# Optimization experiments

Hardware: AMD Instinct MI355X
Metric: run time of the kernel (lower is better)

## Reference

```python
import jax, jax.numpy as jnp
import numpy as np

B, T, C = 4, 2048, 1024
N_HEAD = 16
HEAD = C // N_HEAD  # 64


def _rope_tables(T, dim, base=10000.0):
    inv_freq = 1.0 / (base ** (jnp.arange(0, dim, 2, dtype=jnp.float32) / dim))
    t = jnp.arange(T, dtype=jnp.float32)
    freqs = jnp.einsum('i,j->ij', t, inv_freq)           # [T, dim/2]
    emb = jnp.concatenate([freqs, freqs], axis=-1)        # [T, dim]
    return jnp.cos(emb), jnp.sin(emb)                     # each [T, dim]


def _rotate_half(x):
    x1, x2 = x[..., : x.shape[-1] // 2], x[..., x.shape[-1] // 2:]
    return jnp.concatenate([-x2, x1], axis=-1)


def setup_inputs() -> dict:
    key = jax.random.key(0)
    ks = jax.random.split(key, 4)
    x = jax.random.normal(ks[0], (B, T, C), dtype=jnp.float32)
    w_attn = jax.random.normal(ks[1], (C, 3 * C), dtype=jnp.float32) * (1.0 / np.sqrt(C))
    b_attn = jnp.zeros((3 * C,), dtype=jnp.float32)
    w_proj = jax.random.normal(ks[2], (C, C), dtype=jnp.float32) * (1.0 / np.sqrt(C))
    b_proj = jnp.zeros((C,), dtype=jnp.float32)
    return {"x": x, "w_attn": w_attn, "b_attn": b_attn, "w_proj": w_proj, "b_proj": b_proj}


def reference(x, w_attn, b_attn, w_proj, b_proj):
    Bx, Tx, Cx = x.shape
    qkv = x @ w_attn + b_attn                             # [B,T,3C]
    q, k, v = jnp.split(qkv, 3, axis=-1)
    # [B,T,C] -> [B,H,T,hd]
    def to_heads(t):
        return t.reshape(Bx, Tx, N_HEAD, HEAD).transpose(0, 2, 1, 3)
    q, k, v = to_heads(q), to_heads(k), to_heads(v)
    cos, sin = _rope_tables(Tx, HEAD)                     # [T,hd]
    cos = cos[None, None, :, :]
    sin = sin[None, None, :, :]
    q = q * cos + _rotate_half(q) * sin
    k = k * cos + _rotate_half(k) * sin
    scale = 1.0 / np.sqrt(HEAD)
    att = jnp.einsum('bhqd,bhkd->bhqk', q, k) * scale     # [B,H,T,T]
    causal = jnp.tril(jnp.ones((Tx, Tx), dtype=bool))
    att = jnp.where(causal[None, None], att, -jnp.inf)
    att = jax.nn.softmax(att, axis=-1)
    y = jnp.einsum('bhqk,bhkd->bhqd', att, v)             # [B,H,T,hd]
    y = y.transpose(0, 2, 1, 3).reshape(Bx, Tx, Cx)
    return y @ w_proj + b_proj
```

## Files before the change

kernel.cpp:

```cpp
#include <hip/hip_runtime.h>

#define B_  4
#define T_  2048
#define C_  1024
#define NH_ 16
#define HD_ 64
#define BT_ (B_*T_)
#define N3C (3*C_)

typedef _Float16 f16;
typedef _Float16 half8 __attribute__((ext_vector_type(8)));
typedef _Float16 half4 __attribute__((ext_vector_type(4)));
typedef _Float16 half2v __attribute__((ext_vector_type(2)));
typedef float f32x4 __attribute__((ext_vector_type(4)));

__device__ __forceinline__ void gld16(const f16* g, f16* l) {
  __builtin_amdgcn_global_load_lds(
      (const __attribute__((address_space(1))) unsigned int*)g,
      (__attribute__((address_space(3))) unsigned int*)l, 16, 0, 0);
}

__device__ __forceinline__ float fast_exp2(float x) {
#if __has_builtin(__builtin_amdgcn_exp2f)
  return __builtin_amdgcn_exp2f(x);
#else
  return exp2f(x);
#endif
}

__device__ __forceinline__ half2v cvt_pk_f16(float a, float b) {
#if __has_builtin(__builtin_amdgcn_cvt_pkrtz)
  return __builtin_bit_cast(half2v, __builtin_amdgcn_cvt_pkrtz(a, b));
#else
  half2v r; r[0] = (f16)a; r[1] = (f16)b; return r;
#endif
}

__global__ __launch_bounds__(256) void prep(
    const float* __restrict__ X, f16* __restrict__ X16,
    const float* __restrict__ Wa, f16* __restrict__ Wta,
    const float* __restrict__ Wp, f16* __restrict__ Wtp,
    float2* __restrict__ cs)
{
  __shared__ float Ls[64][65];
  const int tid = threadIdx.x;
  const int blk = blockIdx.x;
  if (blk < 4096) {
    const int i = blk * 256 + tid;
    const float4 a = ((const float4*)X)[i * 2];
    const float4 b = ((const float4*)X)[i * 2 + 1];
    half8 hx;
    hx[0] = (f16)a.x; hx[1] = (f16)a.y; hx[2] = (f16)a.z; hx[3] = (f16)a.w;
    hx[4] = (f16)b.x; hx[5] = (f16)b.y; hx[6] = (f16)b.z; hx[7] = (f16)b.w;
    ((half8*)X16)[i] = hx;
    return;
  }
  if (blk >= 5120) {
    const int i = (blk - 5120) * 256 + tid;
    const int f = i & 31, t = i >> 5;
    const float inv = expf(-(2.0f * (float)f / 64.0f) * 9.210340371976184f);
    float sn, cn;
    sincosf((float)t * inv, &sn, &cn);
    cs[i] = make_float2(cn, sn);
    return;
  }
  const float* W; f16* Wt; int N, i2;
  if (blk < 4864) { W = Wa; Wt = Wta; N = N3C; i2 = blk - 4096; }
  else            { W = Wp; Wt = Wtp; N = C_;  i2 = blk - 4864; }
  const int nblk = N >> 6;
  const int n0 = (i2 % nblk) * 64, k0 = (i2 / nblk) * 64;
#pragma unroll
  for (int j = 0; j < 4; ++j) {
    const int idx = j * 256 + tid;
    const int r = idx >> 4, c = (idx & 15) * 4;
    const float4 w = *(const float4*)(W + (size_t)(k0 + r) * N + n0 + c);
    Ls[r][c + 0] = w.x; Ls[r][c + 1] = w.y; Ls[r][c + 2] = w.z; Ls[r][c + 3] = w.w;
  }
  __syncthreads();
#pragma unroll
  for (int j = 0; j < 2; ++j) {
    const int idx = j * 256 + tid;
    const int r = idx >> 3, c = (idx & 7) * 8;
    half8 hw;
#pragma unroll
    for (int u = 0; u < 8; ++u) hw[u] = (f16)Ls[c + u][r];
    *(half8*)(Wt + (size_t)(n0 + r) * C_ + k0 + c) = hw;
  }
}

__global__ __launch_bounds__(256) void gemm_qkv(
    const f16* __restrict__ A, const f16* __restrict__ Bt,
    const float* __restrict__ bias, const float2* __restrict__ cs,
    f16* __restrict__ Qo, f16* __restrict__ Ko, f16* __restrict__ Vt_g)
{
  __shared__ f16 S[16384];
  f16* As = S;
  f16* Bs = S + 8192;
  const int tid  = threadIdx.x;
  const int row0 = blockIdx.y * 128;
  const int col0 = blockIdx.x * 128;
  const int wave = tid >> 6, lane = tid & 63;
  const int l = lane & 15, quad = lane >> 4;
  const int wm = wave >> 1, wn = wave & 1;
  const int sr = tid >> 3;
  const int scs = ((tid & 7) ^ (sr & 7)) * 8;
  const int lq7 = l & 7;

  f32x4 acc[4][4];
#pragma unroll
  for (int mi = 0; mi < 4; ++mi)
#pragma unroll
    for (int ni = 0; ni < 4; ++ni) acc[mi][ni] = (f32x4)0.0f;

  for (int k0 = 0; k0 < C_; k0 += 64) {
    __syncthreads();
#pragma unroll
    for (int p = 0; p < 4; ++p) {
      const int r = p * 32 + sr;
      gld16(A  + (size_t)(row0 + r) * C_ + k0 + scs, &As[p * 2048 + tid * 8]);
      gld16(Bt + (size_t)(col0 + r) * C_ + k0 + scs, &Bs[p * 2048 + tid * 8]);
    }
    __syncthreads();

#pragma unroll
    for (int s = 0; s < 2; ++s) {
      half8 af[4], bf[4];
#pragma unroll
      for (int mi = 0; mi < 4; ++mi)
        af[mi] = *(const half8*)&As[(wm * 64 + mi * 16 + l) * 64 + ((((s << 2) | quad) ^ lq7) << 3)];
#pragma unroll
      for (int ni = 0; ni < 4; ++ni)
        bf[ni] = *(const half8*)&Bs[(wn * 64 + ni * 16 + l) * 64 + ((((s << 2) | quad) ^ lq7) << 3)];
#pragma unroll
      for (int mi = 0; mi < 4; ++mi)
#pragma unroll
        for (int ni = 0; ni < 4; ++ni)
          acc[mi][ni] = __builtin_amdgcn_mfma_f32_16x16x32_f16(af[mi], bf[ni], acc[mi][ni], 0, 0, 0);
    }
  }

  const int region = col0 >> 10;
  const int colw = col0 + wn * 64;
  const int h = (colw & 1023) >> 6;
  if (region < 2) {
    f16* dst = (region == 0) ? Qo : Ko;
    const float qs = (region == 0) ? 0.18033688f : 1.0f;
#pragma unroll
    for (int mi = 0; mi < 4; ++mi) {
#pragma unroll
      for (int r = 0; r < 4; ++r) {
        const int gm = row0 + wm * 64 + mi * 16 + quad * 4 + r;
        const int b = gm >> 11, t = gm & (T_ - 1);
        const size_t base = ((size_t)(b * NH_ + h) * T_ + t) * HD_;
        const float2* csrow = cs + t * 32;
#pragma unroll
        for (int ni = 0; ni < 2; ++ni) {
          const int d = ni * 16 + l;
          const float2 c2 = csrow[d];
          const float x1 = acc[mi][ni][r]     + bias[colw + d];
          const float x2 = acc[mi][ni + 2][r] + bias[colw + d + 32];
          dst[base + d]      = (f16)((x1 * c2.x - x2 * c2.y) * qs);
          dst[base + d + 32] = (f16)((x2 * c2.x + x1 * c2.y) * qs);
        }
      }
    }
  } else {
    __syncthreads();
    const int bloc  = row0 >> 11;
    const int tbase = row0 & (T_ - 1);
#pragma unroll
    for (int mi = 0; mi < 4; ++mi) {
      const int t_loc = wm * 64 + mi * 16 + quad * 4;
#pragma unroll
      for (int ni = 0; ni < 4; ++ni) {
        const int d = ni * 16 + l;
        const float bs = bias[colw + d];
        half4 o;
#pragma unroll
        for (int r = 0; r < 4; ++r) o[r] = (f16)(acc[mi][ni][r] + bs);
        const int ts = t_loc ^ ((d & 15) << 3);
        *(half4*)&S[wn * 8192 + d * 128 + ts] = o;
      }
    }
    __syncthreads();
#pragma unroll
    for (int j = 0; j < 8; ++j) {
      const int flat = j * 256 + tid;
      const int buf  = flat >> 10;
      const int rem  = flat & 1023;
      const int d    = rem >> 4;
      const int tt   = (rem & 15) << 3;
      const half8 v  = *(const half8*)&S[buf * 8192 + d * 128 + (tt ^ ((d & 15) << 3))];
      const int hh   = ((col0 + buf * 64) & 1023) >> 6;
      *(half8*)(Vt_g + ((size_t)((bloc * NH_ + hh) * HD_ + d)) * T_ + tbase + tt) = v;
    }
  }
}

__global__ __launch_bounds__(256) void attn_mfma(
    const f16* __restrict__ Qg, const f16* __restrict__ Kg,
    const f16* __restrict__ Vt_g, f16* __restrict__ Y)
{
  __shared__ f16 Ks[2][64 * 64];
  __shared__ f16 Vt[2][64 * 64];
  const int tid  = threadIdx.x;
  const int w    = (blockIdx.x & 7) * 128 + (blockIdx.x >> 3);
  const int bh   = w >> 4;
  const int pr   = w & 15;
  const int b    = bh >> 4, h = bh & 15;
  const int wave = tid >> 6, lane = tid & 63;
  const int l    = lane & 15, quad = lane >> 4;
  const int lq7  = l & 7;
  const int r0   = tid >> 3, cc = tid & 7;

  const f16* kbase  = Kg   + (size_t)bh * T_ * HD_;
  const f16* vtbase = Vt_g + (size_t)bh * HD_ * T_;

  const int qts[2] = { 31 - pr, pr };

#pragma unroll 1
  for (int pass = 0; pass < 2; ++pass) {
    const int qt   = qts[pass];
    const int nkt  = qt + 1;
    const int qrow = qt * 64 + wave * 16 + l;

    half8 qf[2];
    {
      const f16* qp = Qg + ((size_t)bh * T_ + qrow) * HD_;
      qf[0] = *(const half8*)(qp + quad * 8);
      qf[1] = *(const half8*)(qp + 32 + quad * 8);
    }

    f32x4 O[4];
#pragma unroll
    for (int mi = 0; mi < 4; ++mi) O[mi] = (f32x4)0.0f;
    float l_run = 0.f;
    const f32x4 zz = (f32x4)0.0f;

    half8 hk[2], hv[2];
#pragma unroll
    for (int i = 0; i < 2; ++i) {
      const int r = i * 32 + r0;
      hk[i] = *(const half8*)(kbase + (size_t)r * HD_ + cc * 8);
      hv[i] = *(const half8*)(vtbase + (size_t)r * T_ + cc * 8);
    }

    if (pass == 1) __syncthreads();

    for (int kt = 0; kt < nkt; ++kt) {
      f16* KsB = Ks[kt & 1];
      f16* VtB = Vt[kt & 1];
#pragma unroll
      for (int i = 0; i < 2; ++i) {
        const int r = i * 32 + r0;
        const int cst = ((cc ^ (r & 7)) << 3);
        *(half8*)&KsB[r * 64 + cst] = hk[i];
        *(half8*)&VtB[r * 64 + cst] = hv[i];
      }
      __syncthreads();
      if (kt + 1 < nkt) {
#pragma unroll
        for (int i = 0; i < 2; ++i) {
          const int r = i * 32 + r0;
          hk[i] = *(const half8*)(kbase + (size_t)((kt + 1) * 64 + r) * HD_ + cc * 8);
          hv[i] = *(const half8*)(vtbase + (size_t)r * T_ + (kt + 1) * 64 + cc * 8);
        }
      }

      f32x4 St[4];
#pragma unroll
      for (int st = 0; st < 4; ++st) {
        const int row = st * 16 + l;
        const half8 af0 = *(const half8*)&KsB[row * 64 + (((quad) ^ lq7) << 3)];
        St[st] = __builtin_amdgcn_mfma_f32_16x16x32_f16(af0, qf[0], zz, 0, 0, 0);
        const half8 af1 = *(const half8*)&KsB[row * 64 + (((4 | quad) ^ lq7) << 3)];
        St[st] = __builtin_amdgcn_mfma_f32_16x16x32_f16(af1, qf[1], St[st], 0, 0, 0);
      }

      const bool domask = (kt == qt);
      const int k0 = kt * 64;
      half4 pf[4];
      float psum = 0.f;
#pragma unroll
      for (int st = 0; st < 4; ++st) {
        float pv[4];
#pragma unroll
        for (int r = 0; r < 4; ++r) {
          float x = St[st][r];
          if (domask) {
            const int key = k0 + st * 16 + quad * 4 + r;
            if (key > qrow) x = -1e9f;
          }
          const float ev = fast_exp2(x);
          pv[r] = ev;
          psum += ev;
        }
        const half2v lo = cvt_pk_f16(pv[0], pv[1]);
        const half2v hi = cvt_pk_f16(pv[2], pv[3]);
        pf[st][0] = lo[0]; pf[st][1] = lo[1];
        pf[st][2] = hi[0]; pf[st][3] = hi[1];
      }
      l_run += psum;

#pragma unroll
      for (int mi = 0; mi < 4; ++mi) {
        const int row = mi * 16 + l;
#pragma unroll
        for (int ki = 0; ki < 4; ++ki) {
          const int kch = (ki << 1) | (quad >> 1);
          const half4 vf = *(const half4*)&VtB[row * 64 + ((kch ^ lq7) << 3) + ((quad & 1) << 2)];
          O[mi] = __builtin_amdgcn_mfma_f32_16x16x16f16(vf, pf[ki], O[mi], 0, 0, 0);
        }
      }
    }

    float lt = l_run;
    lt += __shfl_xor(lt, 16);
    lt += __shfl_xor(lt, 32);
    const float inv = 1.0f / lt;
    f16* yp = Y + ((size_t)(b * T_) + qrow) * C_ + h * 64;
#pragma unroll
    for (int mi = 0; mi < 4; ++mi) {
      half4 o;
      o[0] = (f16)(O[mi][0] * inv); o[1] = (f16)(O[mi][1] * inv);
      o[2] = (f16)(O[mi][2] * inv); o[3] = (f16)(O[mi][3] * inv);
      *(half4*)(yp + mi * 16 + quad * 4) = o;
    }
  }
}

__global__ __launch_bounds__(256) void gemm_proj(
    const f16* __restrict__ A, const f16* __restrict__ Bt,
    const float* __restrict__ bias, float* __restrict__ Out)
{
  __shared__ f16 As[128 * 64];
  __shared__ f16 Bs[128 * 64];
  const int tid  = threadIdx.x;
  const int row0 = blockIdx.y * 128;
  const int col0 = blockIdx.x * 128;
  const int wave = tid >> 6, lane = tid & 63;
  const int l = lane & 15, quad = lane >> 4;
  const int wm = wave >> 1, wn = wave & 1;
  const int sr = tid >> 3;
  const int scs = ((tid & 7) ^ (sr & 7)) * 8;
  const int lq7 = l & 7;

  f32x4 acc[4][4];
#pragma unroll
  for (int mi = 0; mi < 4; ++mi)
#pragma unroll
    for (int ni = 0; ni < 4; ++ni) acc[mi][ni] = (f32x4)0.0f;

  for (int k0 = 0; k0 < C_; k0 += 64) {
    __syncthreads();
#pragma unroll
    for (int p = 0; p < 4; ++p) {
      const int r = p * 32 + sr;
      gld16(A  + (size_t)(row0 + r) * C_ + k0 + scs, &As[p * 2048 + tid * 8]);
      gld16(Bt + (size_t)(col0 + r) * C_ + k0 + scs, &Bs[p * 2048 + tid * 8]);
    }
    __syncthreads();

#pragma unroll
    for (int s = 0; s < 2; ++s) {
      half8 af[4], bf[4];
#pragma unroll
      for (int mi = 0; mi < 4; ++mi)
        af[mi] = *(const half8*)&As[(wm * 64 + mi * 16 + l) * 64 + ((((s << 2) | quad) ^ lq7) << 3)];
#pragma unroll
      for (int ni = 0; ni < 4; ++ni)
        bf[ni] = *(const half8*)&Bs[(wn * 64 + ni * 16 + l) * 64 + ((((s << 2) | quad) ^ lq7) << 3)];
#pragma unroll
      for (int mi = 0; mi < 4; ++mi)
#pragma unroll
        for (int ni = 0; ni < 4; ++ni)
          acc[mi][ni] = __builtin_amdgcn_mfma_f32_16x16x32_f16(af[mi], bf[ni], acc[mi][ni], 0, 0, 0);
    }
  }

#pragma unroll
  for (int mi = 0; mi < 4; ++mi) {
#pragma unroll
    for (int ni = 0; ni < 4; ++ni) {
#pragma unroll
      for (int r = 0; r < 4; ++r) {
        const int gm = row0 + wm * 64 + mi * 16 + quad * 4 + r;
        const int n  = col0 + wn * 64 + ni * 16 + l;
        Out[(size_t)gm * C_ + n] = acc[mi][ni][r] + bias[n];
      }
    }
  }
}

extern "C" void kernel_launch(void* const* d_in, const int* in_sizes, int n_in,
                              void* d_out, int out_size, void* d_ws, size_t ws_size,
                              hipStream_t stream) {
  const float* x      = (const float*)d_in[0];
  const float* w_attn = (const float*)d_in[1];
  const float* b_attn = (const float*)d_in[2];
  const float* w_proj = (const float*)d_in[3];
  const float* b_proj = (const float*)d_in[4];
  float* out = (float*)d_out;

  const size_t elems = (size_t)BT_ * C_;
  f16* x16 = (f16*)d_ws;
  f16* wta = x16 + elems;
  f16* wtp = wta + (size_t)N3C * C_;
  f16* q   = wtp + (size_t)C_ * C_;
  f16* k   = q + elems;
  f16* vt  = k + elems;
  f16* y   = vt + elems;
  float2* cs = (float2*)(y + elems);

  prep<<<dim3(5376), 256, 0, stream>>>(x, x16, w_attn, wta, w_proj, wtp, cs);
  gemm_qkv<<<dim3(N3C / 128, BT_ / 128), 256, 0, stream>>>(x16, wta, b_attn, cs, q, k, vt);
  attn_mfma<<<dim3(1024), 256, 0, stream>>>(q, k, vt, y);
  gemm_proj<<<dim3(C_ / 128, BT_ / 128), 256, 0, stream>>>(y, wtp, b_proj, out);
}
```

Before: 257.0 us.

## Stage Q/K epilogue through LDS for coalesced stores; halve proj GEMM N-tile

```diff
diff --git a/kernel.cpp b/kernel.cpp
--- a/kernel.cpp
+++ b/kernel.cpp
@@ -141,33 +141,45 @@
 
   const int region = col0 >> 10;
   const int colw = col0 + wn * 64;
-  const int h = (colw & 1023) >> 6;
+  const int bloc  = row0 >> 11;
+  const int tbase = row0 & (T_ - 1);
   if (region < 2) {
     f16* dst = (region == 0) ? Qo : Ko;
     const float qs = (region == 0) ? 0.18033688f : 1.0f;
+    __syncthreads();
 #pragma unroll
     for (int mi = 0; mi < 4; ++mi) {
 #pragma unroll
       for (int r = 0; r < 4; ++r) {
-        const int gm = row0 + wm * 64 + mi * 16 + quad * 4 + r;
-        const int b = gm >> 11, t = gm & (T_ - 1);
-        const size_t base = ((size_t)(b * NH_ + h) * T_ + t) * HD_;
-        const float2* csrow = cs + t * 32;
+        const int t = wm * 64 + mi * 16 + quad * 4 + r;
+        const int swz = ((t >> 2) & 3) << 3;
+        const float2* csrow = cs + (tbase + t) * 32;
 #pragma unroll
         for (int ni = 0; ni < 2; ++ni) {
           const int d = ni * 16 + l;
           const float2 c2 = csrow[d];
           const float x1 = acc[mi][ni][r]     + bias[colw + d];
           const float x2 = acc[mi][ni + 2][r] + bias[colw + d + 32];
-          dst[base + d]      = (f16)((x1 * c2.x - x2 * c2.y) * qs);
-          dst[base + d + 32] = (f16)((x2 * c2.x + x1 * c2.y) * qs);
+          S[wn * 8192 + t * 64 + (d ^ swz)]        = (f16)((x1 * c2.x - x2 * c2.y) * qs);
+          S[wn * 8192 + t * 64 + ((d + 32) ^ swz)] = (f16)((x2 * c2.x + x1 * c2.y) * qs);
         }
       }
     }
+    __syncthreads();
+#pragma unroll
+    for (int j = 0; j < 8; ++j) {
+      const int flat = j * 256 + tid;
+      const int wnn  = flat >> 10;
+      const int rem  = flat & 1023;
+      const int t    = rem >> 3;
+      const int d8   = rem & 7;
+      const int swz  = (t >> 2) & 3;
+      const half8 v  = *(const half8*)&S[wnn * 8192 + t * 64 + ((d8 ^ swz) << 3)];
+      const int hh   = ((col0 + wnn * 64) & 1023) >> 6;
+      *(half8*)(dst + ((size_t)(bloc * NH_ + hh) * T_ + tbase + t) * HD_ + d8 * 8) = v;
+    }
   } else {
     __syncthreads();
-    const int bloc  = row0 >> 11;
-    const int tbase = row0 & (T_ - 1);
 #pragma unroll
     for (int mi = 0; mi < 4; ++mi) {
       const int t_loc = wm * 64 + mi * 16 + quad * 4;
@@ -334,10 +346,10 @@
     const float* __restrict__ bias, float* __restrict__ Out)
 {
   __shared__ f16 As[128 * 64];
-  __shared__ f16 Bs[128 * 64];
+  __shared__ f16 Bs[64 * 64];
   const int tid  = threadIdx.x;
   const int row0 = blockIdx.y * 128;
-  const int col0 = blockIdx.x * 128;
+  const int col0 = blockIdx.x * 64;
   const int wave = tid >> 6, lane = tid & 63;
   const int l = lane & 15, quad = lane >> 4;
   const int wm = wave >> 1, wn = wave & 1;
@@ -345,35 +357,39 @@
   const int scs = ((tid & 7) ^ (sr & 7)) * 8;
   const int lq7 = l & 7;
 
-  f32x4 acc[4][4];
+  f32x4 acc[4][2];
 #pragma unroll
   for (int mi = 0; mi < 4; ++mi)
 #pragma unroll
-    for (int ni = 0; ni < 4; ++ni) acc[mi][ni] = (f32x4)0.0f;
+    for (int ni = 0; ni < 2; ++ni) acc[mi][ni] = (f32x4)0.0f;
 
   for (int k0 = 0; k0 < C_; k0 += 64) {
     __syncthreads();
 #pragma unroll
     for (int p = 0; p < 4; ++p) {
       const int r = p * 32 + sr;
-      gld16(A  + (size_t)(row0 + r) * C_ + k0 + scs, &As[p * 2048 + tid * 8]);
+      gld16(A + (size_t)(row0 + r) * C_ + k0 + scs, &As[p * 2048 + tid * 8]);
+    }
+#pragma unroll
+    for (int p = 0; p < 2; ++p) {
+      const int r = p * 32 + sr;
       gld16(Bt + (size_t)(col0 + r) * C_ + k0 + scs, &Bs[p * 2048 + tid * 8]);
     }
     __syncthreads();
 
 #pragma unroll
     for (int s = 0; s < 2; ++s) {
-      half8 af[4], bf[4];
+      half8 af[4], bf[2];
 #pragma unroll
       for (int mi = 0; mi < 4; ++mi)
         af[mi] = *(const half8*)&As[(wm * 64 + mi * 16 + l) * 64 + ((((s << 2) | quad) ^ lq7) << 3)];
 #pragma unroll
-      for (int ni = 0; ni < 4; ++ni)
-        bf[ni] = *(const half8*)&Bs[(wn * 64 + ni * 16 + l) * 64 + ((((s << 2) | quad) ^ lq7) << 3)];
+      for (int ni = 0; ni < 2; ++ni)
+        bf[ni] = *(const half8*)&Bs[(wn * 32 + ni * 16 + l) * 64 + ((((s << 2) | quad) ^ lq7) << 3)];
 #pragma unroll
       for (int mi = 0; mi < 4; ++mi)
 #pragma unroll
-        for (int ni = 0; ni < 4; ++ni)
+        for (int ni = 0; ni < 2; ++ni)
           acc[mi][ni] = __builtin_amdgcn_mfma_f32_16x16x32_f16(af[mi], bf[ni], acc[mi][ni], 0, 0, 0);
     }
   }
@@ -381,11 +397,11 @@
 #pragma unroll
   for (int mi = 0; mi < 4; ++mi) {
 #pragma unroll
-    for (int ni = 0; ni < 4; ++ni) {
+    for (int ni = 0; ni < 2; ++ni) {
 #pragma unroll
       for (int r = 0; r < 4; ++r) {
         const int gm = row0 + wm * 64 + mi * 16 + quad * 4 + r;
-        const int n  = col0 + wn * 64 + ni * 16 + l;
+        const int n  = col0 + wn * 32 + ni * 16 + l;
         Out[(size_t)gm * C_ + n] = acc[mi][ni][r] + bias[n];
       }
     }
@@ -415,5 +431,5 @@
   prep<<<dim3(5376), 256, 0, stream>>>(x, x16, w_attn, wta, w_proj, wtp, cs);
   gemm_qkv<<<dim3(N3C / 128, BT_ / 128), 256, 0, stream>>>(x16, wta, b_attn, cs, q, k, vt);
   attn_mfma<<<dim3(1024), 256, 0, stream>>>(q, k, vt, y);
-  gemm_proj<<<dim3(C_ / 128, BT_ / 128), 256, 0, stream>>>(y, wtp, b_proj, out);
-}
+  gemm_proj<<<dim3(C_ / 64, BT_ / 128), 256, 0, stream>>>(y, wtp, b_proj, out);
+}
```

New measurement: 259.3 us. No clear change (+0.9%).

## Process both paired query tiles concurrently in 512-thread attention blocks; stage Q/K stores through LDS

Applied to the files above, without the earlier changes.

```diff
diff --git a/kernel.cpp b/kernel.cpp
--- a/kernel.cpp
+++ b/kernel.cpp
@@ -141,33 +141,45 @@
 
   const int region = col0 >> 10;
   const int colw = col0 + wn * 64;
-  const int h = (colw & 1023) >> 6;
+  const int bloc  = row0 >> 11;
+  const int tbase = row0 & (T_ - 1);
   if (region < 2) {
     f16* dst = (region == 0) ? Qo : Ko;
     const float qs = (region == 0) ? 0.18033688f : 1.0f;
+    __syncthreads();
 #pragma unroll
     for (int mi = 0; mi < 4; ++mi) {
 #pragma unroll
       for (int r = 0; r < 4; ++r) {
-        const int gm = row0 + wm * 64 + mi * 16 + quad * 4 + r;
-        const int b = gm >> 11, t = gm & (T_ - 1);
-        const size_t base = ((size_t)(b * NH_ + h) * T_ + t) * HD_;
-        const float2* csrow = cs + t * 32;
+        const int t = wm * 64 + mi * 16 + quad * 4 + r;
+        const int swz = ((t >> 2) & 3) << 3;
+        const float2* csrow = cs + (tbase + t) * 32;
 #pragma unroll
         for (int ni = 0; ni < 2; ++ni) {
           const int d = ni * 16 + l;
           const float2 c2 = csrow[d];
           const float x1 = acc[mi][ni][r]     + bias[colw + d];
           const float x2 = acc[mi][ni + 2][r] + bias[colw + d + 32];
-          dst[base + d]      = (f16)((x1 * c2.x - x2 * c2.y) * qs);
-          dst[base + d + 32] = (f16)((x2 * c2.x + x1 * c2.y) * qs);
+          S[wn * 8192 + t * 64 + (d ^ swz)]        = (f16)((x1 * c2.x - x2 * c2.y) * qs);
+          S[wn * 8192 + t * 64 + ((d + 32) ^ swz)] = (f16)((x2 * c2.x + x1 * c2.y) * qs);
         }
       }
     }
+    __syncthreads();
+#pragma unroll
+    for (int j = 0; j < 8; ++j) {
+      const int flat = j * 256 + tid;
+      const int wnn  = flat >> 10;
+      const int rem  = flat & 1023;
+      const int t    = rem >> 3;
+      const int d8   = rem & 7;
+      const int swz  = (t >> 2) & 3;
+      const half8 v  = *(const half8*)&S[wnn * 8192 + t * 64 + ((d8 ^ swz) << 3)];
+      const int hh   = ((col0 + wnn * 64) & 1023) >> 6;
+      *(half8*)(dst + ((size_t)(bloc * NH_ + hh) * T_ + tbase + t) * HD_ + d8 * 8) = v;
+    }
   } else {
     __syncthreads();
-    const int bloc  = row0 >> 11;
-    const int tbase = row0 & (T_ - 1);
 #pragma unroll
     for (int mi = 0; mi < 4; ++mi) {
       const int t_loc = wm * 64 + mi * 16 + quad * 4;
@@ -197,7 +209,7 @@
   }
 }
 
-__global__ __launch_bounds__(256) void attn_mfma(
+__global__ __launch_bounds__(512, 8) void attn_mfma(
     const f16* __restrict__ Qg, const f16* __restrict__ Kg,
     const f16* __restrict__ Vt_g, f16* __restrict__ Y)
 {
@@ -207,66 +219,51 @@
   const int w    = (blockIdx.x & 7) * 128 + (blockIdx.x >> 3);
   const int bh   = w >> 4;
   const int pr   = w & 15;
+  const int qta  = 31 - pr;
+  const int qtb  = pr;
   const int b    = bh >> 4, h = bh & 15;
   const int wave = tid >> 6, lane = tid & 63;
   const int l    = lane & 15, quad = lane >> 4;
   const int lq7  = l & 7;
   const int r0   = tid >> 3, cc = tid & 7;
+  const int u    = wave >> 2, wq = wave & 3;
+  const int qt   = u ? qtb : qta;
+  const int qrow = qt * 64 + wq * 16 + l;
 
   const f16* kbase  = Kg   + (size_t)bh * T_ * HD_;
   const f16* vtbase = Vt_g + (size_t)bh * HD_ * T_;
 
-  const int qts[2] = { 31 - pr, pr };
-
-#pragma unroll 1
-  for (int pass = 0; pass < 2; ++pass) {
-    const int qt   = qts[pass];
-    const int nkt  = qt + 1;
-    const int qrow = qt * 64 + wave * 16 + l;
-
-    half8 qf[2];
-    {
-      const f16* qp = Qg + ((size_t)bh * T_ + qrow) * HD_;
-      qf[0] = *(const half8*)(qp + quad * 8);
-      qf[1] = *(const half8*)(qp + 32 + quad * 8);
-    }
-
-    f32x4 O[4];
-#pragma unroll
-    for (int mi = 0; mi < 4; ++mi) O[mi] = (f32x4)0.0f;
-    float l_run = 0.f;
-    const f32x4 zz = (f32x4)0.0f;
-
-    half8 hk[2], hv[2];
-#pragma unroll
-    for (int i = 0; i < 2; ++i) {
-      const int r = i * 32 + r0;
-      hk[i] = *(const half8*)(kbase + (size_t)r * HD_ + cc * 8);
-      hv[i] = *(const half8*)(vtbase + (size_t)r * T_ + cc * 8);
-    }
-
-    if (pass == 1) __syncthreads();
-
-    for (int kt = 0; kt < nkt; ++kt) {
-      f16* KsB = Ks[kt & 1];
-      f16* VtB = Vt[kt & 1];
-#pragma unroll
-      for (int i = 0; i < 2; ++i) {
-        const int r = i * 32 + r0;
-        const int cst = ((cc ^ (r & 7)) << 3);
-        *(half8*)&KsB[r * 64 + cst] = hk[i];
-        *(half8*)&VtB[r * 64 + cst] = hv[i];
-      }
-      __syncthreads();
-      if (kt + 1 < nkt) {
-#pragma unroll
-        for (int i = 0; i < 2; ++i) {
-          const int r = i * 32 + r0;
-          hk[i] = *(const half8*)(kbase + (size_t)((kt + 1) * 64 + r) * HD_ + cc * 8);
-          hv[i] = *(const half8*)(vtbase + (size_t)r * T_ + (kt + 1) * 64 + cc * 8);
-        }
-      }
-
+  half8 qf[2];
+  {
+    const f16* qp = Qg + ((size_t)bh * T_ + qrow) * HD_;
+    qf[0] = *(const half8*)(qp + quad * 8);
+    qf[1] = *(const half8*)(qp + 32 + quad * 8);
+  }
+
+  f32x4 O[4];
+#pragma unroll
+  for (int mi = 0; mi < 4; ++mi) O[mi] = (f32x4)0.0f;
+  float l_run = 0.f;
+  const f32x4 zz = (f32x4)0.0f;
+
+  half8 hk = *(const half8*)(kbase + (size_t)r0 * HD_ + cc * 8);
+  half8 hv = *(const half8*)(vtbase + (size_t)r0 * T_ + cc * 8);
+
+  const int nkt = qta + 1;
+  const int cst = ((cc ^ (r0 & 7)) << 3);
+
+  for (int kt = 0; kt < nkt; ++kt) {
+    f16* KsB = Ks[kt & 1];
+    f16* VtB = Vt[kt & 1];
+    *(half8*)&KsB[r0 * 64 + cst] = hk;
+    *(half8*)&VtB[r0 * 64 + cst] = hv;
+    __syncthreads();
+    if (kt + 1 < nkt) {
+      hk = *(const half8*)(kbase + (size_t)((kt + 1) * 64 + r0) * HD_ + cc * 8);
+      hv = *(const half8*)(vtbase + (size_t)r0 * T_ + (kt + 1) * 64 + cc * 8);
+    }
+
+    if (u == 0 || kt <= qtb) {
       f32x4 St[4];
 #pragma unroll
       for (int st = 0; st < 4; ++st) {
@@ -313,19 +310,19 @@
         }
       }
     }
-
-    float lt = l_run;
-    lt += __shfl_xor(lt, 16);
-    lt += __shfl_xor(lt, 32);
-    const float inv = 1.0f / lt;
-    f16* yp = Y + ((size_t)(b * T_) + qrow) * C_ + h * 64;
-#pragma unroll
-    for (int mi = 0; mi < 4; ++mi) {
-      half4 o;
-      o[0] = (f16)(O[mi][0] * inv); o[1] = (f16)(O[mi][1] * inv);
-      o[2] = (f16)(O[mi][2] * inv); o[3] = (f16)(O[mi][3] * inv);
-      *(half4*)(yp + mi * 16 + quad * 4) = o;
-    }
+  }
+
+  float lt = l_run;
+  lt += __shfl_xor(lt, 16);
+  lt += __shfl_xor(lt, 32);
+  const float inv = 1.0f / lt;
+  f16* yp = Y + ((size_t)(b * T_) + qrow) * C_ + h * 64;
+#pragma unroll
+  for (int mi = 0; mi < 4; ++mi) {
+    half4 o;
+    o[0] = (f16)(O[mi][0] * inv); o[1] = (f16)(O[mi][1] * inv);
+    o[2] = (f16)(O[mi][2] * inv); o[3] = (f16)(O[mi][3] * inv);
+    *(half4*)(yp + mi * 16 + quad * 4) = o;
   }
 }
 
@@ -414,6 +411,6 @@
 
   prep<<<dim3(5376), 256, 0, stream>>>(x, x16, w_attn, wta, w_proj, wtp, cs);
   gemm_qkv<<<dim3(N3C / 128, BT_ / 128), 256, 0, stream>>>(x16, wta, b_attn, cs, q, k, vt);
-  attn_mfma<<<dim3(1024), 256, 0, stream>>>(q, k, vt, y);
+  attn_mfma<<<dim3(1024), 512, 0, stream>>>(q, k, vt, y);
   gemm_proj<<<dim3(C_ / 128, BT_ / 128), 256, 0, stream>>>(y, wtp, b_proj, out);
 }
```

Result: slower. 331.0 us (+28.8%).
